# Performance work log

Hardware: AMD Instinct MI355X
Metric: run time of the kernel (lower is better)

Reference implementation:

```python
import jax, jax.numpy as jnp
import numpy as np

BN = 1024      # B*N voxel groups
M = 32         # points per voxel
D_MODEL = 128
D_POINTS = 64


def _mlp(x, w1, b1, w2, b2):
    # Linear -> ReLU -> Linear (torch nn.Sequential equivalent)
    return jax.nn.relu(x @ w1 + b1) @ w2 + b2


def setup_inputs() -> dict:
    key = jax.random.key(0)
    ks = jax.random.split(key, 16)
    def lin(k, din, dout):
        return (jax.random.normal(k, (din, dout), jnp.float32) / np.sqrt(din)).astype(jnp.float32)
    inp = {}
    inp["pv_xyz"] = jax.random.normal(ks[0], (BN, M, 3), jnp.float32)
    inp["features"] = jax.random.normal(ks[1], (BN, M, D_POINTS), jnp.float32)
    i = 2
    for name, din in [("alpha", 3), ("beta", 3), ("delta", 3), ("epsilon", D_MODEL), ("omega", D_POINTS)]:
        inp[f"{name}_w1"] = lin(ks[i], din, D_MODEL); i += 1
        inp[f"{name}_b1"] = jnp.zeros((D_MODEL,), jnp.float32)
        inp[f"{name}_w2"] = lin(ks[i], D_MODEL, D_MODEL); i += 1
        inp[f"{name}_b2"] = jnp.zeros((D_MODEL,), jnp.float32)
    return inp


def reference(pv_xyz, features,
              alpha_w1, alpha_b1, alpha_w2, alpha_b2,
              beta_w1, beta_b1, beta_w2, beta_b2,
              delta_w1, delta_b1, delta_w2, delta_b2,
              epsilon_w1, epsilon_b1, epsilon_w2, epsilon_b2,
              omega_w1, omega_b1, omega_w2, omega_b2):
    # abs relative position: [BN, M, M, 3]
    dist = jnp.abs(pv_xyz[:, :, None, :] - pv_xyz[:, None, :, :])
    pij = _mlp(dist, delta_w1, delta_b1, delta_w2, delta_b2)          # [BN,M,M,D]
    q = _mlp(pv_xyz, alpha_w1, alpha_b1, alpha_w2, alpha_b2)          # [BN,M,D]
    k = _mlp(pv_xyz, beta_w1, beta_b1, beta_w2, beta_b2)              # [BN,M,D]
    v = _mlp(features, omega_w1, omega_b1, omega_w2, omega_b2)        # [BN,M,D]
    scale = jnp.float32(1.0 / np.sqrt(D_MODEL))
    w = _mlp((q[:, :, None, :] - k[:, None, :, :] + pij) * scale,
             epsilon_w1, epsilon_b1, epsilon_w2, epsilon_b2)          # [BN,M,M,D]
    wij = jax.nn.softmax(w, axis=-2)                                  # softmax over key axis
    # torch.einsum('bmmf,bmf->bmf', wij, v): repeated index -> diagonal of wij
    midx = jnp.arange(wij.shape[1])
    res = wij[:, midx, midx, :] * v                                   # [BN,M,D]
    return jnp.concatenate([res, features], axis=-1)                  # [BN,M,D+C]
```

## Files before the change

### kernel.cpp

```cpp
#include <hip/hip_runtime.h>
#include <hip/hip_bf16.h>
#include <cstdint>
#include <cstddef>


#define SCALE 0.08838834764831843f

typedef __bf16 bf16x8 __attribute__((ext_vector_type(8)));
typedef float f32x16 __attribute__((ext_vector_type(16)));

__device__ __forceinline__ ushort f2b(float f){
  __hip_bfloat16 h = __float2bfloat16(f);
  return __builtin_bit_cast(ushort, h);
}
__device__ __forceinline__ float b2f(uint32_t s){
  union { uint32_t u; float f; } x; x.u = s << 16; return x.f;
}
__device__ __forceinline__ float blo(uint32_t u){
  union { uint32_t x; float f; } v; v.x = u << 16; return v.f;
}
__device__ __forceinline__ float bhi(uint32_t u){
  union { uint32_t x; float f; } v; v.x = u & 0xffff0000u; return v.f;
}
__device__ __forceinline__ uint32_t pk2(float a, float b){
  union { __hip_bfloat162 h2; uint32_t u; } x;
  x.h2.x = __float2bfloat16(a); x.h2.y = __float2bfloat16(b);
  return x.u;
}
__device__ __forceinline__ f32x16 MFMA(uint4 a, uint4 b, f32x16 c){
  return __builtin_amdgcn_mfma_f32_32x32x16_bf16(
      __builtin_bit_cast(bf16x8, a), __builtin_bit_cast(bf16x8, b), c, 0, 0, 0);
}

__global__ __launch_bounds__(256) void k_pre(
    const float* __restrict__ A2, const float* __restrict__ B2, const float* __restrict__ D2,
    const float* __restrict__ E1, const float* __restrict__ E2,
    const float* __restrict__ O1, const float* __restrict__ O2,
    const float* __restrict__ ab2, const float* __restrict__ bb2, const float* __restrict__ db2,
    const float* __restrict__ eb1,
    const float* __restrict__ D1, const float* __restrict__ db1,
    ushort* __restrict__ aep, ushort* __restrict__ bep, ushort* __restrict__ gtp,
    ushort* __restrict__ e2p, ushort* __restrict__ o2p, ushort* __restrict__ o1t,
    ushort* __restrict__ d1p, float* __restrict__ c0)
{
  const int bid = blockIdx.x, tid = threadIdx.x;
  if (bid < 192){
    const float* W = (bid < 64) ? A2 : (bid < 128) ? B2 : D2;
    ushort* dst    = (bid < 64) ? aep : (bid < 128) ? bep : gtp;
    int flat = (bid & 63)*256 + tid;
    int co = flat >> 10, rem = flat & 1023, h = rem >> 3, i = rem & 7;
    int r = co*8 + i;
    float acc = 0.f;
    for (int t = 0; t < 128; ++t) acc = fmaf(W[r*128 + t], E1[t*128 + h], acc);
    dst[(co*128 + h)*8 + i] = f2b(acc * SCALE);
  } else if (bid < 256){
    int flat = (bid - 192)*256 + tid;
    int co = flat >> 10, rem = flat & 1023, d = rem >> 3, i = rem & 7;
    e2p[(co*128 + d)*8 + i] = f2b(E2[(co*8 + i)*128 + d]);
  } else if (bid < 320){
    int flat = (bid - 256)*256 + tid;
    int co = flat >> 10, rem = flat & 1023, d = rem >> 3, i = rem & 7;
    o2p[(co*128 + d)*8 + i] = f2b(O2[(co*8 + i)*128 + d]);
  } else if (bid < 352){
    int flat = (bid - 320)*256 + tid;
    int fo = flat >> 10, rem = flat & 1023, o = rem >> 3, e = rem & 7;
    o1t[(fo*128 + o)*8 + e] = f2b(O1[(fo*8 + e)*128 + o]);
  } else if (bid < 360){
    int flat = (bid - 352)*256 + tid;
    int koct = flat >> 10, cd = (flat >> 3) & 127, e = flat & 7;
    float val = 0.f;
    if (koct == 0){
      if (e < 3) val = D1[e*128 + cd];
      else if (e == 3) val = db1[cd];
    }
    d1p[flat] = f2b(val);
  } else {
    if (tid < 128){
      float acc = 0.f;
      for (int t = 0; t < 128; ++t) acc = fmaf(ab2[t] - bb2[t] + db2[t], E1[t*128 + tid], acc);
      c0[tid] = acc * SCALE + eb1[tid];
    }
  }
}

__device__ __forceinline__ void gemm64x128(const ushort (*sa)[64][8], const ushort (*sw)[128][8],
                                           int w, int l31, int hl, int p0,
                                           const float* __restrict__ bias,
                                           ushort* __restrict__ dst)
{
  const int rw = w >> 1, ctb = (w & 1) * 2;
  f32x16 acc0, acc1;
#pragma unroll
  for (int r = 0; r < 16; ++r){ acc0[r] = 0.f; acc1[r] = 0.f; }
#pragma unroll
  for (int kk = 0; kk < 8; ++kk){
    uint4 a  = *(const uint4*)&sa[2*kk + hl][32*rw + l31][0];
    uint4 b0 = *(const uint4*)&sw[2*kk + hl][32*ctb + l31][0];
    uint4 b1 = *(const uint4*)&sw[2*kk + hl][32*(ctb+1) + l31][0];
    acc0 = MFMA(a, b0, acc0);
    acc1 = MFMA(a, b1, acc1);
  }
#pragma unroll
  for (int t = 0; t < 2; ++t){
    const f32x16 acc = t ? acc1 : acc0;
    const int d = 32*(ctb + t) + l31;
    const float bv = bias ? bias[d] : 0.f;
#pragma unroll
    for (int r = 0; r < 16; ++r){
      int row = 32*rw + (r & 3) + 8*(r >> 2) + 4*hl;
      dst[(size_t)(p0 + row)*128 + d] = f2b(acc[r] + bv);
    }
  }
}

__global__ __launch_bounds__(256, 2) void k_point(
    const float* __restrict__ pv, const float* __restrict__ feat,
    const float* __restrict__ A1, const float* __restrict__ ab1,
    const float* __restrict__ B1, const float* __restrict__ bb1,
    const float* __restrict__ ob1, const float* __restrict__ ob2,
    const float* __restrict__ c0,
    const uint4* __restrict__ aep, const uint4* __restrict__ bep,
    const uint4* __restrict__ o1t, const uint4* __restrict__ o2p,
    ushort* __restrict__ qe_ws, ushort* __restrict__ ke_ws, ushort* __restrict__ v_ws,
    float* __restrict__ out)
{
  __shared__ ushort sW[16][128][8];
  __shared__ ushort sA[16][64][8];
  __shared__ ushort sF[8][64][8];
  __shared__ float  sLw[3][128];
  __shared__ float  sLb[128];
  __shared__ float  sLb2[128];

  const int tid = threadIdx.x;
  const int p0  = blockIdx.x * 64;
  const int w = tid >> 6, lane = tid & 63, l31 = lane & 31, hl = lane >> 5;

  for (int idx = tid; idx < 64*16; idx += 256){
    int p = idx >> 4, k4 = idx & 15;
    float4 f = ((const float4*)(feat + (size_t)(p0 + p)*64))[k4];
    ((float4*)(out + (size_t)(p0 + p)*192 + 128))[k4] = f;
  }

  for (int idx = tid; idx < 2048; idx += 256) ((uint4*)sW)[idx] = aep[idx];
  for (int idx = tid; idx < 384; idx += 256) ((float*)sLw)[idx] = A1[idx];
  if (tid < 128) sLb[tid] = ab1[tid];
  __syncthreads();
  {
    int p = tid & 63, ob = tid >> 6;
    float x0 = pv[(size_t)(p0+p)*3+0], x1 = pv[(size_t)(p0+p)*3+1], x2 = pv[(size_t)(p0+p)*3+2];
#pragma unroll
    for (int it = 0; it < 4; ++it){
      int oct = ob + 4*it;
      float h[8];
#pragma unroll
      for (int e = 0; e < 8; ++e){
        int cd = oct*8 + e;
        float t = fmaf(x0, sLw[0][cd], fmaf(x1, sLw[1][cd], fmaf(x2, sLw[2][cd], sLb[cd])));
        h[e] = fmaxf(t, 0.f);
      }
      uint4 u; u.x = pk2(h[0],h[1]); u.y = pk2(h[2],h[3]); u.z = pk2(h[4],h[5]); u.w = pk2(h[6],h[7]);
      *(uint4*)&sA[oct][p][0] = u;
    }
  }
  __syncthreads();
  gemm64x128(sA, sW, w, l31, hl, p0, c0, qe_ws);
  __syncthreads();

  for (int idx = tid; idx < 2048; idx += 256) ((uint4*)sW)[idx] = bep[idx];
  for (int idx = tid; idx < 384; idx += 256) ((float*)sLw)[idx] = B1[idx];
  if (tid < 128) sLb[tid] = bb1[tid];
  __syncthreads();
  {
    int p = tid & 63, ob = tid >> 6;
    float x0 = pv[(size_t)(p0+p)*3+0], x1 = pv[(size_t)(p0+p)*3+1], x2 = pv[(size_t)(p0+p)*3+2];
#pragma unroll
    for (int it = 0; it < 4; ++it){
      int oct = ob + 4*it;
      float h[8];
#pragma unroll
      for (int e = 0; e < 8; ++e){
        int cd = oct*8 + e;
        float t = fmaf(x0, sLw[0][cd], fmaf(x1, sLw[1][cd], fmaf(x2, sLw[2][cd], sLb[cd])));
        h[e] = fmaxf(t, 0.f);
      }
      uint4 u; u.x = pk2(h[0],h[1]); u.y = pk2(h[2],h[3]); u.z = pk2(h[4],h[5]); u.w = pk2(h[6],h[7]);
      *(uint4*)&sA[oct][p][0] = u;
    }
  }
  __syncthreads();
  gemm64x128(sA, sW, w, l31, hl, p0, nullptr, ke_ws);
  __syncthreads();

  for (int idx = tid; idx < 512; idx += 256){
    int p = idx & 63, fo = idx >> 6;
    const float* fp = feat + (size_t)(p0 + p)*64 + 8*fo;
    float4 f0 = ((const float4*)fp)[0], f1 = ((const float4*)fp)[1];
    uint4 u; u.x = pk2(f0.x,f0.y); u.y = pk2(f0.z,f0.w); u.z = pk2(f1.x,f1.y); u.w = pk2(f1.z,f1.w);
    *(uint4*)&sF[fo][p][0] = u;
  }
  for (int idx = tid; idx < 1024; idx += 256) ((uint4*)sW)[idx] = o1t[idx];
  if (tid < 128) sLb[tid] = ob1[tid];
  __syncthreads();
  {
    f32x16 acc0, acc1;
#pragma unroll
    for (int r = 0; r < 16; ++r){ acc0[r] = 0.f; acc1[r] = 0.f; }
#pragma unroll
    for (int kk = 0; kk < 4; ++kk){
      uint4 a  = *(const uint4*)&sW[2*kk + hl][32*w + l31][0];
      uint4 b0 = *(const uint4*)&sF[2*kk + hl][l31][0];
      uint4 b1 = *(const uint4*)&sF[2*kk + hl][32 + l31][0];
      acc0 = MFMA(a, b0, acc0);
      acc1 = MFMA(a, b1, acc1);
    }
#pragma unroll
    for (int t = 0; t < 2; ++t){
      const f32x16 acc = t ? acc1 : acc0;
      const int pt = 32*t + l31;
#pragma unroll
      for (int q = 0; q < 4; ++q){
        int o0 = 32*w + 8*q + 4*hl;
        float z0 = fmaxf(acc[4*q+0] + sLb[o0+0], 0.f);
        float z1 = fmaxf(acc[4*q+1] + sLb[o0+1], 0.f);
        float z2 = fmaxf(acc[4*q+2] + sLb[o0+2], 0.f);
        float z3 = fmaxf(acc[4*q+3] + sLb[o0+3], 0.f);
        uint2 u; u.x = pk2(z0, z1); u.y = pk2(z2, z3);
        *(uint2*)&sA[4*w + q][pt][4*hl] = u;
      }
    }
  }
  __syncthreads();

  for (int idx = tid; idx < 2048; idx += 256) ((uint4*)sW)[idx] = o2p[idx];
  if (tid < 128) sLb2[tid] = ob2[tid];
  __syncthreads();
  {
    const int rw = w >> 1, ctb = (w & 1) * 2;
    f32x16 acc0, acc1;
#pragma unroll
    for (int r = 0; r < 16; ++r){ acc0[r] = 0.f; acc1[r] = 0.f; }
#pragma unroll
    for (int kk = 0; kk < 8; ++kk){
      uint4 a  = *(const uint4*)&sA[2*kk + hl][32*rw + l31][0];
      uint4 b0 = *(const uint4*)&sW[2*kk + hl][32*ctb + l31][0];
      uint4 b1 = *(const uint4*)&sW[2*kk + hl][32*(ctb+1) + l31][0];
      acc0 = MFMA(a, b0, acc0);
      acc1 = MFMA(a, b1, acc1);
    }
#pragma unroll
    for (int t = 0; t < 2; ++t){
      const f32x16 acc = t ? acc1 : acc0;
      const int d = 32*(ctb + t) + l31;
      const float bias = sLb2[d];
#pragma unroll
      for (int r = 0; r < 16; ++r){
        int row = 32*rw + (r & 3) + 8*(r >> 2) + 4*hl;
        v_ws[(size_t)(p0 + row)*128 + d] = f2b(acc[r] + bias);
      }
    }
  }
}

__global__ __launch_bounds__(256, 3) void k_main(
    const float* __restrict__ pv,
    const ushort* __restrict__ qe_ws, const ushort* __restrict__ ke_ws, const ushort* __restrict__ v_ws,
    const uint4* __restrict__ gtp, const uint4* __restrict__ e2p, const uint4* __restrict__ d1p,
    float* __restrict__ out)
{
  __shared__ ushort sHDE[16][128][8];
  __shared__ ushort sQE[16][128];
  __shared__ float  sXYZ[32][3];

  const int tid = threadIdx.x;
  const int b   = blockIdx.x >> 1;
  const int ch0 = (blockIdx.x & 1) * 4;
  const int w = tid >> 6, lane = tid & 63, l31 = lane & 31, hl = lane >> 5;

  for (int idx = tid; idx < 96; idx += 256) ((float*)sXYZ)[idx] = pv[(size_t)b*96 + idx];
  for (int idx = tid; idx < 512; idx += 256)
    ((uint2*)sQE)[idx] = ((const uint2*)qe_ws)[(size_t)(b*32 + 4*ch0)*32 + idx];

  float kreg[16];
  {
    const ushort* kp = ke_ws + (size_t)(b*32 + l31)*128 + 32*w + 4*hl;
#pragma unroll
    for (int q = 0; q < 4; ++q){
      uint2 ku = *(const uint2*)(kp + 8*q);
      kreg[4*q+0] = b2f(ku.x & 0xffff); kreg[4*q+1] = b2f(ku.x >> 16);
      kreg[4*q+2] = b2f(ku.y & 0xffff); kreg[4*q+3] = b2f(ku.y >> 16);
    }
  }
  uint4 wG[8], wE[8];
#pragma unroll
  for (int kk = 0; kk < 8; ++kk){
    wG[kk] = gtp[(2*kk + hl)*128 + 32*w + l31];
    wE[kk] = e2p[(2*kk + hl)*128 + 32*w + l31];
  }
  uint4 wD = d1p[hl*128 + 32*w + l31];
  __syncthreads();

  const float xj0 = sXYZ[l31][0], xj1 = sXYZ[l31][1], xj2 = sXYZ[l31][2];

#pragma unroll
  for (int cc = 0; cc < 4; ++cc){
    const int c = ch0 + cc;

    f32x16 accD[4];
#pragma unroll
    for (int ct = 0; ct < 4; ++ct){
      const int i = 4*c + ct;
      float dx = fabsf(sXYZ[i][0] - xj0);
      float dy = fabsf(sXYZ[i][1] - xj1);
      float dz = fabsf(sXYZ[i][2] - xj2);
      uint4 bD; bD.x = pk2(dx, dy); bD.y = pk2(dz, 1.0f); bD.z = 0u; bD.w = 0u;
      f32x16 z;
#pragma unroll
      for (int r = 0; r < 16; ++r) z[r] = 0.f;
      accD[ct] = MFMA(wD, bD, z);
    }
#pragma unroll
    for (int ct = 0; ct < 4; ++ct){
#pragma unroll
      for (int q = 0; q < 4; ++q){
        uint2 o;
        o.x = pk2(fmaxf(accD[ct][4*q+0],0.f), fmaxf(accD[ct][4*q+1],0.f));
        o.y = pk2(fmaxf(accD[ct][4*q+2],0.f), fmaxf(accD[ct][4*q+3],0.f));
        *(uint2*)&sHDE[4*w + q][32*ct + l31][4*hl] = o;
      }
    }
    __syncthreads();

    f32x16 acc1[4];
#pragma unroll
    for (int ct = 0; ct < 4; ++ct){
      const int il = 4*cc + ct;
#pragma unroll
      for (int q = 0; q < 4; ++q){
        uint2 qu = *(const uint2*)&sQE[il][32*w + 4*hl + 8*q];
        acc1[ct][4*q+0] = blo(qu.x) - kreg[4*q+0];
        acc1[ct][4*q+1] = bhi(qu.x) - kreg[4*q+1];
        acc1[ct][4*q+2] = blo(qu.y) - kreg[4*q+2];
        acc1[ct][4*q+3] = bhi(qu.y) - kreg[4*q+3];
      }
    }
#pragma unroll
    for (int kk = 0; kk < 8; ++kk){
      uint4 a = wG[kk];
#pragma unroll
      for (int ct = 0; ct < 4; ++ct){
        uint4 bu = *(const uint4*)&sHDE[2*kk + hl][32*ct + l31][0];
        acc1[ct] = MFMA(a, bu, acc1[ct]);
      }
    }
    __syncthreads();

#pragma unroll
    for (int ct = 0; ct < 4; ++ct){
#pragma unroll
      for (int q = 0; q < 4; ++q){
        uint2 o;
        o.x = pk2(fmaxf(acc1[ct][4*q+0],0.f), fmaxf(acc1[ct][4*q+1],0.f));
        o.y = pk2(fmaxf(acc1[ct][4*q+2],0.f), fmaxf(acc1[ct][4*q+3],0.f));
        *(uint2*)&sHDE[4*w + q][32*ct + l31][4*hl] = o;
      }
    }
    __syncthreads();

    float vv[4];
#pragma unroll
    for (int rt = 0; rt < 4; ++rt)
      vv[rt] = b2f((uint32_t)v_ws[(size_t)(b*32 + 4*c + rt)*128 + 32*w + l31]);

    f32x16 acc2[4];
#pragma unroll
    for (int rt = 0; rt < 4; ++rt)
#pragma unroll
      for (int r = 0; r < 16; ++r) acc2[rt][r] = 0.f;
#pragma unroll
    for (int kk = 0; kk < 8; ++kk){
      uint4 bfrag = wE[kk];
#pragma unroll
      for (int rt = 0; rt < 4; ++rt){
        uint4 au = *(const uint4*)&sHDE[2*kk + hl][32*rt + l31][0];
        acc2[rt] = MFMA(au, bfrag, acc2[rt]);
      }
    }

    const int g = (c >> 1) & 3;
    const int hls = c & 1;
#pragma unroll
    for (int rt = 0; rt < 4; ++rt){
      float e[16];
#pragma unroll
      for (int r = 0; r < 16; ++r) e[r] = __expf(acc2[rt][r]);
      float s01 = e[0]+e[1],   s23 = e[2]+e[3],   s45 = e[4]+e[5],   s67 = e[6]+e[7];
      float s89 = e[8]+e[9],   sab = e[10]+e[11], scd = e[12]+e[13], sef = e[14]+e[15];
      float s = ((s01+s23)+(s45+s67)) + ((s89+sab)+(scd+sef));
      s += __shfl_xor(s, 32);
      float num = (g == 0) ? e[rt] : (g == 1) ? e[rt+4] : (g == 2) ? e[rt+8] : e[rt+12];
      if (hl == hls){
        out[(size_t)(b*32 + 4*c + rt)*192 + 32*w + l31] = num * __builtin_amdgcn_rcpf(s) * vv[rt];
      }
    }
    __syncthreads();
  }
}

static constexpr size_t OFF_AEP = 0;
static constexpr size_t OFF_BEP = 32768;
static constexpr size_t OFF_GTP = 65536;
static constexpr size_t OFF_E2P = 98304;
static constexpr size_t OFF_O1T = 131072;
static constexpr size_t OFF_O2P = 147456;
static constexpr size_t OFF_C0  = 180224;
static constexpr size_t OFF_D1P = 180736;
static constexpr size_t OFF_QE  = 184832;
static constexpr size_t OFF_KE  = OFF_QE + (size_t)32768*128*2;
static constexpr size_t OFF_V   = OFF_KE + (size_t)32768*128*2;

extern "C" void kernel_launch(void* const* d_in, const int* in_sizes, int n_in,
                              void* d_out, int out_size, void* d_ws, size_t ws_size,
                              hipStream_t stream)
{
  (void)in_sizes; (void)n_in; (void)out_size; (void)ws_size;
  const float* pv   = (const float*)d_in[0];
  const float* feat = (const float*)d_in[1];
  const float* A1 = (const float*)d_in[2];  const float* ab1 = (const float*)d_in[3];
  const float* A2 = (const float*)d_in[4];  const float* ab2 = (const float*)d_in[5];
  const float* B1 = (const float*)d_in[6];  const float* bb1 = (const float*)d_in[7];
  const float* B2 = (const float*)d_in[8];  const float* bb2 = (const float*)d_in[9];
  const float* D1 = (const float*)d_in[10]; const float* db1 = (const float*)d_in[11];
  const float* D2 = (const float*)d_in[12]; const float* db2 = (const float*)d_in[13];
  const float* E1 = (const float*)d_in[14]; const float* eb1 = (const float*)d_in[15];
  const float* E2 = (const float*)d_in[16];
  const float* O1 = (const float*)d_in[18]; const float* ob1 = (const float*)d_in[19];
  const float* O2 = (const float*)d_in[20]; const float* ob2 = (const float*)d_in[21];

  char* ws = (char*)d_ws;
  ushort* aep = (ushort*)(ws + OFF_AEP);
  ushort* bep = (ushort*)(ws + OFF_BEP);
  ushort* gtp = (ushort*)(ws + OFF_GTP);
  ushort* e2p = (ushort*)(ws + OFF_E2P);
  ushort* o1t = (ushort*)(ws + OFF_O1T);
  ushort* o2p = (ushort*)(ws + OFF_O2P);
  float*  c0  = (float*)(ws + OFF_C0);
  ushort* d1p = (ushort*)(ws + OFF_D1P);
  ushort* qe  = (ushort*)(ws + OFF_QE);
  ushort* ke  = (ushort*)(ws + OFF_KE);
  ushort* vv  = (ushort*)(ws + OFF_V);
  float* out = (float*)d_out;

  hipLaunchKernelGGL(k_pre, dim3(361), dim3(256), 0, stream,
                     A2, B2, D2, E1, E2, O1, O2, ab2, bb2, db2, eb1, D1, db1,
                     aep, bep, gtp, e2p, o2p, o1t, d1p, c0);
  hipLaunchKernelGGL(k_point, dim3(512), dim3(256), 0, stream,
                     pv, feat, A1, ab1, B1, bb1, ob1, ob2, c0,
                     (const uint4*)aep, (const uint4*)bep, (const uint4*)o1t, (const uint4*)o2p,
                     qe, ke, vv, out);
  hipLaunchKernelGGL(k_main, dim3(2048), dim3(256), 0, stream,
                     pv, qe, ke, vv, (const uint4*)gtp, (const uint4*)e2p, (const uint4*)d1p,
                     out);
}
```

Measured before the change: 120.2 us.

## Retile k_main into a 2x2 warp grid with double-buffered LDS

k_main now runs one block per voxel group instead of two and loops over all 8 query chunks. Warps are arranged as a 2x2 grid so each MFMA B/A fragment read from LDS feeds two accumulators. The hidden activation uses separate pA/pB buffers, so the next chunk's delta-MLP layer can be computed while the current chunk finishes, which drops one barrier per chunk. The softmax exp becomes a native exp2 with log2e folded into the E2 weights. In exchange the grid is halved, register use rises and launch bounds drop to 2 blocks per CU, so fewer waves are resident.

Result: slower. 125.6 us (+4.5%).

```diff
diff --git a/kernel.cpp b/kernel.cpp
--- a/kernel.cpp
+++ b/kernel.cpp
@@ -5,6 +5,7 @@
 
 
 #define SCALE 0.08838834764831843f
+#define LOG2E 1.4426950408889634f
 
 typedef __bf16 bf16x8 __attribute__((ext_vector_type(8)));
 typedef float f32x16 __attribute__((ext_vector_type(16)));
@@ -56,7 +57,7 @@
   } else if (bid < 256){
     int flat = (bid - 192)*256 + tid;
     int co = flat >> 10, rem = flat & 1023, d = rem >> 3, i = rem & 7;
-    e2p[(co*128 + d)*8 + i] = f2b(E2[(co*8 + i)*128 + d]);
+    e2p[(co*128 + d)*8 + i] = f2b(E2[(co*8 + i)*128 + d] * LOG2E);
   } else if (bid < 320){
     int flat = (bid - 256)*256 + tid;
     int co = flat >> 10, rem = flat & 1023, d = rem >> 3, i = rem & 7;
@@ -261,147 +262,161 @@
   }
 }
 
-__global__ __launch_bounds__(256, 3) void k_main(
+__global__ __launch_bounds__(256, 2) void k_main(
     const float* __restrict__ pv,
     const ushort* __restrict__ qe_ws, const ushort* __restrict__ ke_ws, const ushort* __restrict__ v_ws,
     const uint4* __restrict__ gtp, const uint4* __restrict__ e2p, const uint4* __restrict__ d1p,
     float* __restrict__ out)
 {
-  __shared__ ushort sHDE[16][128][8];
-  __shared__ ushort sQE[16][128];
+  __shared__ ushort pA[16][128][8];
+  __shared__ ushort pB[16][128][8];
+  __shared__ ushort sQE[32][128];
   __shared__ float  sXYZ[32][3];
 
   const int tid = threadIdx.x;
-  const int b   = blockIdx.x >> 1;
-  const int ch0 = (blockIdx.x & 1) * 4;
+  const int b   = blockIdx.x;
   const int w = tid >> 6, lane = tid & 63, l31 = lane & 31, hl = lane >> 5;
+  const int wm = w >> 1, wn = w & 1;
 
   for (int idx = tid; idx < 96; idx += 256) ((float*)sXYZ)[idx] = pv[(size_t)b*96 + idx];
   for (int idx = tid; idx < 512; idx += 256)
-    ((uint2*)sQE)[idx] = ((const uint2*)qe_ws)[(size_t)(b*32 + 4*ch0)*32 + idx];
-
-  float kreg[16];
-  {
-    const ushort* kp = ke_ws + (size_t)(b*32 + l31)*128 + 32*w + 4*hl;
-#pragma unroll
-    for (int q = 0; q < 4; ++q){
-      uint2 ku = *(const uint2*)(kp + 8*q);
-      kreg[4*q+0] = b2f(ku.x & 0xffff); kreg[4*q+1] = b2f(ku.x >> 16);
-      kreg[4*q+2] = b2f(ku.y & 0xffff); kreg[4*q+3] = b2f(ku.y >> 16);
-    }
-  }
-  uint4 wG[8], wE[8];
+    ((uint4*)sQE)[idx] = ((const uint4*)(qe_ws + (size_t)b*32*128))[idx];
+
+  uint2 kp[2][4];
+#pragma unroll
+  for (int a = 0; a < 2; ++a)
+#pragma unroll
+    for (int q = 0; q < 4; ++q)
+      kp[a][q] = *(const uint2*)(ke_ws + (size_t)(b*32 + l31)*128 + 64*wm + 32*a + 4*hl + 8*q);
+
+  uint4 wG[2][8], wE[2][8];
 #pragma unroll
   for (int kk = 0; kk < 8; ++kk){
-    wG[kk] = gtp[(2*kk + hl)*128 + 32*w + l31];
-    wE[kk] = e2p[(2*kk + hl)*128 + 32*w + l31];
+#pragma unroll
+    for (int a = 0; a < 2; ++a){
+      wG[a][kk] = gtp[(2*kk + hl)*128 + 64*wm + 32*a + l31];
+      wE[a][kk] = e2p[(2*kk + hl)*128 + 64*wn + 32*a + l31];
+    }
   }
   uint4 wD = d1p[hl*128 + 32*w + l31];
   __syncthreads();
 
   const float xj0 = sXYZ[l31][0], xj1 = sXYZ[l31][1], xj2 = sXYZ[l31][2];
 
-#pragma unroll
-  for (int cc = 0; cc < 4; ++cc){
-    const int c = ch0 + cc;
-
-    f32x16 accD[4];
+  auto hdgen = [&](int cn){
+    f32x16 Z;
+#pragma unroll
+    for (int r = 0; r < 16; ++r) Z[r] = 0.f;
 #pragma unroll
     for (int ct = 0; ct < 4; ++ct){
-      const int i = 4*c + ct;
+      const int i = 4*cn + ct;
       float dx = fabsf(sXYZ[i][0] - xj0);
       float dy = fabsf(sXYZ[i][1] - xj1);
       float dz = fabsf(sXYZ[i][2] - xj2);
       uint4 bD; bD.x = pk2(dx, dy); bD.y = pk2(dz, 1.0f); bD.z = 0u; bD.w = 0u;
-      f32x16 z;
-#pragma unroll
-      for (int r = 0; r < 16; ++r) z[r] = 0.f;
-      accD[ct] = MFMA(wD, bD, z);
-    }
-#pragma unroll
-    for (int ct = 0; ct < 4; ++ct){
+      f32x16 t = MFMA(wD, bD, Z);
 #pragma unroll
       for (int q = 0; q < 4; ++q){
         uint2 o;
-        o.x = pk2(fmaxf(accD[ct][4*q+0],0.f), fmaxf(accD[ct][4*q+1],0.f));
-        o.y = pk2(fmaxf(accD[ct][4*q+2],0.f), fmaxf(accD[ct][4*q+3],0.f));
-        *(uint2*)&sHDE[4*w + q][32*ct + l31][4*hl] = o;
-      }
-    }
+        o.x = pk2(fmaxf(t[4*q+0],0.f), fmaxf(t[4*q+1],0.f));
+        o.y = pk2(fmaxf(t[4*q+2],0.f), fmaxf(t[4*q+3],0.f));
+        *(uint2*)&pA[4*w + q][32*ct + l31][4*hl] = o;
+      }
+    }
+  };
+
+  hdgen(0);
+  __syncthreads();
+
+  for (int cc = 0; cc < 8; ++cc){
+    f32x16 acc[2][2];
+
+#pragma unroll
+    for (int a = 0; a < 2; ++a){
+#pragma unroll
+      for (int q = 0; q < 4; ++q){
+        float k0 = blo(kp[a][q].x), k1 = bhi(kp[a][q].x);
+        float k2 = blo(kp[a][q].y), k3 = bhi(kp[a][q].y);
+#pragma unroll
+        for (int bb = 0; bb < 2; ++bb){
+          uint2 qu = *(const uint2*)&sQE[4*cc + 2*wn + bb][64*wm + 32*a + 4*hl + 8*q];
+          acc[a][bb][4*q+0] = blo(qu.x) - k0;
+          acc[a][bb][4*q+1] = bhi(qu.x) - k1;
+          acc[a][bb][4*q+2] = blo(qu.y) - k2;
+          acc[a][bb][4*q+3] = bhi(qu.y) - k3;
+        }
+      }
+    }
+#pragma unroll
+    for (int kk = 0; kk < 8; ++kk){
+      uint4 b0 = *(const uint4*)&pA[2*kk + hl][32*(2*wn+0) + l31][0];
+      uint4 b1 = *(const uint4*)&pA[2*kk + hl][32*(2*wn+1) + l31][0];
+      acc[0][0] = MFMA(wG[0][kk], b0, acc[0][0]);
+      acc[0][1] = MFMA(wG[0][kk], b1, acc[0][1]);
+      acc[1][0] = MFMA(wG[1][kk], b0, acc[1][0]);
+      acc[1][1] = MFMA(wG[1][kk], b1, acc[1][1]);
+    }
+#pragma unroll
+    for (int a = 0; a < 2; ++a)
+#pragma unroll
+      for (int bb = 0; bb < 2; ++bb)
+#pragma unroll
+        for (int q = 0; q < 4; ++q){
+          uint2 o;
+          o.x = pk2(fmaxf(acc[a][bb][4*q+0],0.f), fmaxf(acc[a][bb][4*q+1],0.f));
+          o.y = pk2(fmaxf(acc[a][bb][4*q+2],0.f), fmaxf(acc[a][bb][4*q+3],0.f));
+          *(uint2*)&pB[8*wm + 4*a + q][32*(2*wn+bb) + l31][4*hl] = o;
+        }
     __syncthreads();
 
-    f32x16 acc1[4];
-#pragma unroll
-    for (int ct = 0; ct < 4; ++ct){
-      const int il = 4*cc + ct;
-#pragma unroll
-      for (int q = 0; q < 4; ++q){
-        uint2 qu = *(const uint2*)&sQE[il][32*w + 4*hl + 8*q];
-        acc1[ct][4*q+0] = blo(qu.x) - kreg[4*q+0];
-        acc1[ct][4*q+1] = bhi(qu.x) - kreg[4*q+1];
-        acc1[ct][4*q+2] = blo(qu.y) - kreg[4*q+2];
-        acc1[ct][4*q+3] = bhi(qu.y) - kreg[4*q+3];
-      }
-    }
+    float vv[2][2];
+#pragma unroll
+    for (int a = 0; a < 2; ++a)
+#pragma unroll
+      for (int bb = 0; bb < 2; ++bb)
+        vv[a][bb] = b2f((uint32_t)v_ws[(size_t)(b*32 + 4*cc + 2*wm + a)*128 + 64*wn + 32*bb + l31]);
+
+#pragma unroll
+    for (int a = 0; a < 2; ++a)
+#pragma unroll
+      for (int bb = 0; bb < 2; ++bb)
+#pragma unroll
+        for (int r = 0; r < 16; ++r) acc[a][bb][r] = 0.f;
 #pragma unroll
     for (int kk = 0; kk < 8; ++kk){
-      uint4 a = wG[kk];
-#pragma unroll
-      for (int ct = 0; ct < 4; ++ct){
-        uint4 bu = *(const uint4*)&sHDE[2*kk + hl][32*ct + l31][0];
-        acc1[ct] = MFMA(a, bu, acc1[ct]);
-      }
-    }
-    __syncthreads();
-
-#pragma unroll
-    for (int ct = 0; ct < 4; ++ct){
-#pragma unroll
-      for (int q = 0; q < 4; ++q){
-        uint2 o;
-        o.x = pk2(fmaxf(acc1[ct][4*q+0],0.f), fmaxf(acc1[ct][4*q+1],0.f));
-        o.y = pk2(fmaxf(acc1[ct][4*q+2],0.f), fmaxf(acc1[ct][4*q+3],0.f));
-        *(uint2*)&sHDE[4*w + q][32*ct + l31][4*hl] = o;
-      }
-    }
-    __syncthreads();
-
-    float vv[4];
-#pragma unroll
-    for (int rt = 0; rt < 4; ++rt)
-      vv[rt] = b2f((uint32_t)v_ws[(size_t)(b*32 + 4*c + rt)*128 + 32*w + l31]);
-
-    f32x16 acc2[4];
-#pragma unroll
-    for (int rt = 0; rt < 4; ++rt)
-#pragma unroll
-      for (int r = 0; r < 16; ++r) acc2[rt][r] = 0.f;
-#pragma unroll
-    for (int kk = 0; kk < 8; ++kk){
-      uint4 bfrag = wE[kk];
-#pragma unroll
-      for (int rt = 0; rt < 4; ++rt){
-        uint4 au = *(const uint4*)&sHDE[2*kk + hl][32*rt + l31][0];
-        acc2[rt] = MFMA(au, bfrag, acc2[rt]);
-      }
-    }
-
-    const int g = (c >> 1) & 3;
-    const int hls = c & 1;
-#pragma unroll
-    for (int rt = 0; rt < 4; ++rt){
-      float e[16];
-#pragma unroll
-      for (int r = 0; r < 16; ++r) e[r] = __expf(acc2[rt][r]);
-      float s01 = e[0]+e[1],   s23 = e[2]+e[3],   s45 = e[4]+e[5],   s67 = e[6]+e[7];
-      float s89 = e[8]+e[9],   sab = e[10]+e[11], scd = e[12]+e[13], sef = e[14]+e[15];
-      float s = ((s01+s23)+(s45+s67)) + ((s89+sab)+(scd+sef));
-      s += __shfl_xor(s, 32);
-      float num = (g == 0) ? e[rt] : (g == 1) ? e[rt+4] : (g == 2) ? e[rt+8] : e[rt+12];
-      if (hl == hls){
-        out[(size_t)(b*32 + 4*c + rt)*192 + 32*w + l31] = num * __builtin_amdgcn_rcpf(s) * vv[rt];
-      }
-    }
+      uint4 a0 = *(const uint4*)&pB[2*kk + hl][32*(2*wm+0) + l31][0];
+      uint4 a1 = *(const uint4*)&pB[2*kk + hl][32*(2*wm+1) + l31][0];
+      acc[0][0] = MFMA(a0, wE[0][kk], acc[0][0]);
+      acc[0][1] = MFMA(a0, wE[1][kk], acc[0][1]);
+      acc[1][0] = MFMA(a1, wE[0][kk], acc[1][0]);
+      acc[1][1] = MFMA(a1, wE[1][kk], acc[1][1]);
+    }
+
+    const int g = cc >> 1, hls = cc & 1;
+#pragma unroll
+    for (int a = 0; a < 2; ++a){
+#pragma unroll
+      for (int bb = 0; bb < 2; ++bb){
+#pragma unroll
+        for (int r = 0; r < 16; ++r) acc[a][bb][r] = __builtin_amdgcn_exp2f(acc[a][bb][r]);
+        float s = ((acc[a][bb][0]+acc[a][bb][1]) + (acc[a][bb][2]+acc[a][bb][3]))
+                + ((acc[a][bb][4]+acc[a][bb][5]) + (acc[a][bb][6]+acc[a][bb][7]))
+                + ((acc[a][bb][8]+acc[a][bb][9]) + (acc[a][bb][10]+acc[a][bb][11]))
+                + ((acc[a][bb][12]+acc[a][bb][13]) + (acc[a][bb][14]+acc[a][bb][15]));
+        s += __shfl_xor(s, 32);
+        float c0v = wm ? acc[a][bb][2+a+0]  : acc[a][bb][a+0];
+        float c1v = wm ? acc[a][bb][2+a+4]  : acc[a][bb][a+4];
+        float c2v = wm ? acc[a][bb][2+a+8]  : acc[a][bb][a+8];
+        float c3v = wm ? acc[a][bb][2+a+12] : acc[a][bb][a+12];
+        float num = (g == 0) ? c0v : (g == 1) ? c1v : (g == 2) ? c2v : c3v;
+        if (hl == hls){
+          const int i = 4*cc + 2*wm + a;
+          out[(size_t)(b*32 + i)*192 + 64*wn + 32*bb + l31] = num * __builtin_amdgcn_rcpf(s) * vv[a][bb];
+        }
+      }
+    }
+
+    if (cc < 7) hdgen(cc + 1);
     __syncthreads();
   }
 }
@@ -457,7 +472,7 @@
                      pv, feat, A1, ab1, B1, bb1, ob1, ob2, c0,
                      (const uint4*)aep, (const uint4*)bep, (const uint4*)o1t, (const uint4*)o2p,
                      qe, ke, vv, out);
-  hipLaunchKernelGGL(k_main, dim3(2048), dim3(256), 0, stream,
+  hipLaunchKernelGGL(k_main, dim3(1024), dim3(256), 0, stream,
                      pv, qe, ke, vv, (const uint4*)gtp, (const uint4*)e2p, (const uint4*)d1p,
                      out);
 }
```
